# Kernel optimization log

Measured on AMD Instinct MI355X. Metric: run time of the kernel, lower is better.

The kernel has to match this reference:

```python
import jax, jax.numpy as jnp
import numpy as np
import math

N, B, C, H = 197, 256, 768, 12
HEAD = C // H
DROP_RATE = 0.5  # forward-arg drop_rate, hardcoded (float scalar)


def setup_inputs() -> dict:
    key = jax.random.key(0)
    ks = jax.random.split(key, 6)
    s = lambda k, shape: jax.random.normal(k, shape, jnp.float32) * 0.02
    return dict(
        x=jax.random.normal(ks[0], (N, B, C), jnp.float32),
        ln1_g=jnp.ones((C,), jnp.float32), ln1_b=jnp.zeros((C,), jnp.float32),
        in_proj_w=s(ks[1], (3 * C, C)), in_proj_b=jnp.zeros((3 * C,), jnp.float32),
        out_proj_w=s(ks[2], (C, C)), out_proj_b=jnp.zeros((C,), jnp.float32),
        ln2_g=jnp.ones((C,), jnp.float32), ln2_b=jnp.zeros((C,), jnp.float32),
        fc_w=s(ks[3], (4 * C, C)), fc_b=jnp.zeros((4 * C,), jnp.float32),
        proj_w=s(ks[4], (C, 4 * C)), proj_b=jnp.zeros((C,), jnp.float32),
    )


def layernorm(x, g, b, eps=1e-5):
    x32 = x.astype(jnp.float32)
    mu = x32.mean(-1, keepdims=True)
    var = x32.var(-1, keepdims=True)
    return ((x32 - mu) * jax.lax.rsqrt(var + eps) * g + b).astype(x.dtype)


def quick_gelu(x):
    return x * jax.nn.sigmoid(1.702 * x)


def mha(x, w, b, ow, ob):
    # x: (N, B, C); torch nn.MultiheadAttention with need_weights=True,
    # average_attn_weights=False -> weights (B, H, N, N)
    qkv = jnp.einsum('nbc,dc->nbd', x, w) + b
    q, k, v = jnp.split(qkv, 3, axis=-1)
    heads = lambda t: t.reshape(t.shape[0], B, H, HEAD).transpose(1, 2, 0, 3)  # (B,H,N,hd)
    q, k, v = heads(q), heads(k), heads(v)
    scale = 1.0 / np.sqrt(HEAD).astype(np.float32)
    scores = jnp.einsum('bhqd,bhkd->bhqk', q, k) * scale
    attn_w = jax.nn.softmax(scores, axis=-1)  # (B, H, N, N)
    o = jnp.einsum('bhqk,bhkd->bhqd', attn_w, v)
    o = o.transpose(2, 0, 1, 3).reshape(x.shape[0], B, C)
    return jnp.einsum('nbc,dc->nbd', o, ow) + ob, attn_w


def evit_block(x, ln1_g, ln1_b, in_proj_w, in_proj_b, out_proj_w, out_proj_b,
               ln2_g, ln2_b, fc_w, fc_b, proj_w, proj_b):
    L = math.ceil((1.0 - DROP_RATE) * (N - 1))  # left_tokens
    tmp, attn_w = mha(layernorm(x, ln1_g, ln1_b), in_proj_w, in_proj_b, out_proj_w, out_proj_b)
    x = x + tmp
    cls_attn = attn_w[:, :, 0, 1:].mean(axis=1)  # (B, N-1): CLS->patch attn, head-avg
    _, idx = jax.lax.top_k(cls_attn, L)          # (B, L), sorted descending like torch.topk
    nb = x[1:].transpose(1, 0, 2)                # (B, N-1, C) non-cls tokens, batch-first
    x_others = jnp.take_along_axis(nb, idx[:, :, None], axis=1)  # (B, L, C)
    # complement_idx: arange, zero out topk positions, sort, drop first L entries
    a = jnp.broadcast_to(jnp.arange(N - 1), (B, N - 1))
    mask = jnp.zeros((B, N - 1), bool).at[jnp.arange(B)[:, None], idx].set(True)
    compl = jnp.sort(jnp.where(mask, 0, a), axis=1)[:, L:]       # (B, N-1-L)
    non_topk = jnp.take_along_axis(nb, compl[:, :, None], axis=1)      # (B, M, C)
    non_topk_attn = jnp.take_along_axis(cls_attn, compl, axis=1)       # (B, M)
    extra = jnp.sum(non_topk * non_topk_attn[:, :, None], axis=1)      # (B, C) weighted merge
    x_new = jnp.concatenate([x[:1], x_others.transpose(1, 0, 2), extra[None]], axis=0)  # (L+2,B,C)
    h = layernorm(x_new, ln2_g, ln2_b)
    h = quick_gelu(jnp.einsum('nbc,fc->nbf', h, fc_w) + fc_b)
    h = jnp.einsum('nbf,cf->nbc', h, proj_w) + proj_b
    return x_new + h


def reference(x, ln1_g, ln1_b, in_proj_w, in_proj_b, out_proj_w, out_proj_b,
              ln2_g, ln2_b, fc_w, fc_b, proj_w, proj_b):
    return evit_block(x, ln1_g, ln1_b, in_proj_w, in_proj_b, out_proj_w, out_proj_b,
                      ln2_g, ln2_b, fc_w, fc_b, proj_w, proj_b)
```

## Files before the change

### kernel.cpp

```cpp
#include <hip/hip_runtime.h>
#include <math.h>

#define NT   197
#define BB   256
#define CD   768
#define NHD  12
#define HD   64
#define LTK  98
#define NEWN 100
#define M1   (NT*BB)
#define M2   (NEWN*BB)

typedef __attribute__((ext_vector_type(8))) short short8;
typedef __attribute__((ext_vector_type(4))) float float4v;

__device__ __forceinline__ short f2bf(float f) {
    unsigned int u = __float_as_uint(f);
    u = (u + 0x7fffu + ((u >> 16) & 1u)) >> 16;
    return (short)u;
}

__device__ __forceinline__ void global_to_lds16(const short* g, short* l) {
    __builtin_amdgcn_global_load_lds(
        (__attribute__((address_space(1))) void*)(void*)g,
        (__attribute__((address_space(3))) void*)l, 16, 0, 0);
}

__global__ __launch_bounds__(256) void cvt_bf16(const float* __restrict__ s,
                                                short* __restrict__ d, int n) {
    int i = blockIdx.x * 256 + threadIdx.x;
    if (i < n) d[i] = f2bf(s[i]);
}

__global__ __launch_bounds__(256)
void ln_fwd(const float* __restrict__ x, const float* __restrict__ g,
            const float* __restrict__ bb, short* __restrict__ ob,
            float2* __restrict__ stats) {
    int row = blockIdx.x * 4 + (threadIdx.x >> 6);
    int lane = threadIdx.x & 63;
    const float* xr = x + (size_t)row * CD;
    float v[12]; float s = 0.f;
#pragma unroll
    for (int i = 0; i < 12; i++) { v[i] = xr[lane + i * 64]; s += v[i]; }
#pragma unroll
    for (int o = 32; o; o >>= 1) s += __shfl_xor(s, o);
    float mu = s * (1.f / 768.f);
    float s2 = 0.f;
#pragma unroll
    for (int i = 0; i < 12; i++) { float d = v[i] - mu; s2 += d * d; }
#pragma unroll
    for (int o = 32; o; o >>= 1) s2 += __shfl_xor(s2, o);
    float rsig = rsqrtf(s2 * (1.f / 768.f) + 1e-5f);
    if (stats != nullptr && lane == 0) stats[row] = make_float2(mu, rsig);
#pragma unroll
    for (int i = 0; i < 12; i++) {
        int c = lane + i * 64;
        ob[(size_t)row * CD + c] = f2bf((v[i] - mu) * rsig * g[c] + bb[c]);
    }
}

template <int EPI>
__global__ __launch_bounds__(512)
void gemm_bt(const short* __restrict__ A, const short* __restrict__ Bw,
             const float* __restrict__ bias, const float* __restrict__ res,
             void* __restrict__ out, int M, int Nd, int K) {
    __shared__ short As[256 * 32];
    __shared__ short Bs[128 * 32];
    const int tid = threadIdx.x;

    const int mTiles = M >> 8, nTiles = Nd >> 7;
    const int GM = 8;
    int per = GM * nTiles;
    int grp = blockIdx.x / per;
    int rem = blockIdx.x - grp * per;
    int gm = mTiles - grp * GM; if (gm > GM) gm = GM;
    int mt = grp * GM + rem % gm;
    int nt = rem / gm;
    const int m0 = mt * 256, n0 = nt * 128;

    const int wave = tid >> 6, lane = tid & 63;
    const int wm = wave >> 1, wn = wave & 1;

    float4v acc[4][4];
#pragma unroll
    for (int a = 0; a < 4; a++)
#pragma unroll
        for (int b = 0; b < 4; b++) acc[a][b] = (float4v){0.f, 0.f, 0.f, 0.f};

    const int r = lane & 15, q = lane >> 4;

    for (int k0 = 0; k0 < K; k0 += 32) {
#pragma unroll
        for (int i = 0; i < 2; i++) {
            int id = (wave * 2 + i) * 64 + lane;
            int row = id >> 2, cpos = id & 3;
            int csrc = cpos ^ ((row >> 1) & 3);
            global_to_lds16(A + (size_t)(m0 + row) * K + k0 + csrc * 8,
                            As + (wave * 2 + i) * 512);
        }
        {
            int id = wave * 64 + lane;
            int row = id >> 2, cpos = id & 3;
            int csrc = cpos ^ ((row >> 1) & 3);
            global_to_lds16(Bw + (size_t)(n0 + row) * K + k0 + csrc * 8,
                            Bs + wave * 512);
        }
        __syncthreads();
        short8 af[4], bf[4];
#pragma unroll
        for (int mi = 0; mi < 4; mi++) {
            int row = wm * 64 + mi * 16 + r;
            int cp = q ^ ((row >> 1) & 3);
            af[mi] = *(const short8*)(As + row * 32 + cp * 8);
        }
#pragma unroll
        for (int ni = 0; ni < 4; ni++) {
            int row = wn * 64 + ni * 16 + r;
            int cp = q ^ ((row >> 1) & 3);
            bf[ni] = *(const short8*)(Bs + row * 32 + cp * 8);
        }
#pragma unroll
        for (int mi = 0; mi < 4; mi++)
#pragma unroll
            for (int ni = 0; ni < 4; ni++)
                acc[mi][ni] = __builtin_amdgcn_mfma_f32_16x16x32_bf16(
                    af[mi], bf[ni], acc[mi][ni], 0, 0, 0);
        __syncthreads();
    }

#pragma unroll
    for (int ni = 0; ni < 4; ni++) {
        int col = n0 + wn * 64 + ni * 16 + r;
        float bv = bias[col];
#pragma unroll
        for (int mi = 0; mi < 4; mi++) {
#pragma unroll
            for (int r2 = 0; r2 < 4; r2++) {
                int row = m0 + wm * 64 + mi * 16 + q * 4 + r2;
                size_t off = (size_t)row * Nd + col;
                float v = acc[mi][ni][r2] + bv;
                if (EPI == 0) {
                    ((short*)out)[off] = f2bf(v);
                } else if (EPI == 1) {
                    ((float*)out)[off] = v + res[off];
                } else {
                    float gel = v / (1.f + __expf(-1.702f * v));
                    ((short*)out)[off] = f2bf(gel);
                }
            }
        }
    }
}

__global__ __launch_bounds__(448)
void attn_kernel(const short* __restrict__ qkv, short* __restrict__ o) {
    __shared__ short Ks[224 * 72];
    __shared__ short Vt[64 * 232];
    __shared__ short Ps[7 * 16 * 232];

    const int b = blockIdx.x / NHD, h = blockIdx.x % NHD;
    const int tid = threadIdx.x;
    const int wave = tid >> 6, lane = tid & 63;

#pragma unroll
    for (int i = 0; i < 4; i++) {
        int id = tid + 448 * i;
        int n = id >> 3, ch = id & 7;
        uint4 val = {0u, 0u, 0u, 0u};
        if (n < NT)
            val = *(const uint4*)(qkv + ((size_t)(n * BB + b) * 2304 + 768 + h * 64 + ch * 8));
        *(uint4*)(&Ks[n * 72 + ch * 8]) = val;
    }
#pragma unroll
    for (int rr = 0; rr < 8; rr++) {
        int p = (tid >> 5) + rr * 14;
        int dl = tid & 31;
        int n0p = 2 * p;
#pragma unroll
        for (int di = 0; di < 2; di++) {
            int d = dl + 32 * di;
            unsigned int pack = 0;
            if (n0p < NT)
                pack |= (unsigned int)*(const unsigned short*)(qkv +
                    ((size_t)(n0p * BB + b) * 2304 + 1536 + h * 64 + d));
            if (n0p + 1 < NT)
                pack |= ((unsigned int)*(const unsigned short*)(qkv +
                    ((size_t)((n0p + 1) * BB + b) * 2304 + 1536 + h * 64 + d))) << 16;
            *(unsigned int*)(&Vt[d * 232 + n0p]) = pack;
        }
    }
    __syncthreads();

    short* Ps_w = Ps + wave * 16 * 232;
    const int cl = lane & 15, qg = lane >> 4;

    for (int rep = 0; rep < 2; rep++) {
        int qt = wave + rep * 7;
        int q0 = qt * 16;
        int m = q0 + cl; int mrow = (m < NT) ? m : (NT - 1);
        short8 qf[2];
#pragma unroll
        for (int kk = 0; kk < 2; kk++)
            qf[kk] = *(const short8*)(qkv + ((size_t)(mrow * BB + b) * 2304 +
                                             h * 64 + kk * 32 + qg * 8));
        float4v sacc[14];
#pragma unroll
        for (int nt = 0; nt < 14; nt++) sacc[nt] = (float4v){0.f, 0.f, 0.f, 0.f};
#pragma unroll
        for (int kk = 0; kk < 2; kk++) {
#pragma unroll
            for (int nt = 0; nt < 14; nt++) {
                short8 kf = *(const short8*)(&Ks[(nt * 16 + cl) * 72 + kk * 32 + qg * 8]);
                sacc[nt] = __builtin_amdgcn_mfma_f32_16x16x32_bf16(qf[kk], kf, sacc[nt], 0, 0, 0);
            }
        }
        float mx[4] = {-1e30f, -1e30f, -1e30f, -1e30f};
#pragma unroll
        for (int nt = 0; nt < 14; nt++) {
            int col = nt * 16 + cl;
            bool valid = col < NT;
#pragma unroll
            for (int r2 = 0; r2 < 4; r2++) {
                if (!valid) sacc[nt][r2] = -1e30f;
                mx[r2] = fmaxf(mx[r2], sacc[nt][r2]);
            }
        }
#pragma unroll
        for (int o2 = 1; o2 < 16; o2 <<= 1)
#pragma unroll
            for (int r2 = 0; r2 < 4; r2++) mx[r2] = fmaxf(mx[r2], __shfl_xor(mx[r2], o2));
        float sm[4] = {0.f, 0.f, 0.f, 0.f};
#pragma unroll
        for (int nt = 0; nt < 14; nt++)
#pragma unroll
            for (int r2 = 0; r2 < 4; r2++) {
                float pv = __expf((sacc[nt][r2] - mx[r2]) * 0.125f);
                sacc[nt][r2] = pv; sm[r2] += pv;
            }
#pragma unroll
        for (int o2 = 1; o2 < 16; o2 <<= 1)
#pragma unroll
            for (int r2 = 0; r2 < 4; r2++) sm[r2] += __shfl_xor(sm[r2], o2);
        float inv[4];
#pragma unroll
        for (int r2 = 0; r2 < 4; r2++) inv[r2] = 1.f / sm[r2];
#pragma unroll
        for (int nt = 0; nt < 14; nt++) {
            int col = nt * 16 + cl;
#pragma unroll
            for (int r2 = 0; r2 < 4; r2++)
                Ps_w[(qg * 4 + r2) * 232 + col] = f2bf(sacc[nt][r2] * inv[r2]);
        }
        __syncthreads();
        float4v oacc[4];
#pragma unroll
        for (int dt = 0; dt < 4; dt++) oacc[dt] = (float4v){0.f, 0.f, 0.f, 0.f};
#pragma unroll
        for (int kk = 0; kk < 7; kk++) {
            short8 pf = *(const short8*)(&Ps_w[cl * 232 + kk * 32 + qg * 8]);
#pragma unroll
            for (int dt = 0; dt < 4; dt++) {
                short8 vf = *(const short8*)(&Vt[(dt * 16 + cl) * 232 + kk * 32 + qg * 8]);
                oacc[dt] = __builtin_amdgcn_mfma_f32_16x16x32_bf16(pf, vf, oacc[dt], 0, 0, 0);
            }
        }
#pragma unroll
        for (int dt = 0; dt < 4; dt++)
#pragma unroll
            for (int r2 = 0; r2 < 4; r2++) {
                int qrow = q0 + qg * 4 + r2;
                if (qrow < NT)
                    o[((size_t)qrow * BB + b) * CD + h * 64 + dt * 16 + cl] = f2bf(oacc[dt][r2]);
            }
        __syncthreads();
    }
}

__global__ __launch_bounds__(256)
void u_kernel(const float* __restrict__ x, const float2* __restrict__ stats,
              const float* __restrict__ g, const float* __restrict__ bln,
              const float* __restrict__ W, const float* __restrict__ pb,
              float* __restrict__ u, float* __restrict__ tq) {
    int b = blockIdx.x;
    __shared__ float lncls[CD];
    __shared__ float qc[CD];
    float2 st = stats[b];
    for (int c = threadIdx.x; c < CD; c += 256)
        lncls[c] = (x[(size_t)b * CD + c] - st.x) * st.y * g[c] + bln[c];
    __syncthreads();
    for (int d = threadIdx.x; d < CD; d += 256) {
        const float* wr = W + (size_t)d * CD;
        float acc = 0.f;
        for (int c = 0; c < CD; c++) acc += wr[c] * lncls[c];
        qc[d] = acc + pb[d];
    }
    __syncthreads();
    for (int t = threadIdx.x; t < NHD * CD; t += 256) {
        int h = t / CD, c = t % CD;
        const float* wk = W + (size_t)(CD + h * 64) * CD + c;
        float acc = 0.f;
        for (int d = 0; d < 64; d++) acc += qc[h * 64 + d] * wk[(size_t)d * CD];
        u[((size_t)b * NHD + h) * CD + c] = acc;
    }
    if (threadIdx.x < NHD) {
        int h = threadIdx.x; float acc = 0.f;
        for (int d = 0; d < 64; d++) acc += qc[h * 64 + d] * pb[CD + h * 64 + d];
        tq[b * NHD + h] = acc;
    }
}

__global__ __launch_bounds__(256)
void scores_kernel(const float* __restrict__ x, const float2* __restrict__ stats,
                   const float* __restrict__ g, const float* __restrict__ bln,
                   const float* __restrict__ u, const float* __restrict__ tq,
                   float* __restrict__ scores) {
    int bi = blockIdx.x; int b = bi / NT, n = bi % NT;
    __shared__ float ln[CD];
    int row = n * BB + b;
    float2 st = stats[row];
    for (int c = threadIdx.x; c < CD; c += 256)
        ln[c] = (x[(size_t)row * CD + c] - st.x) * st.y * g[c] + bln[c];
    __syncthreads();
    int wave = threadIdx.x >> 6, lane = threadIdx.x & 63;
    for (int h = wave; h < NHD; h += 4) {
        const float* ub = u + ((size_t)b * NHD + h) * CD;
        float acc = 0.f;
#pragma unroll
        for (int i = 0; i < 12; i++) acc += ub[lane + i * 64] * ln[lane + i * 64];
#pragma unroll
        for (int o2 = 32; o2; o2 >>= 1) acc += __shfl_xor(acc, o2);
        if (lane == 0)
            scores[((size_t)b * NHD + h) * NT + n] = (acc + tq[b * NHD + h]) * 0.125f;
    }
}

__global__ __launch_bounds__(256)
void softmax_avg(const float* __restrict__ scores, float* __restrict__ cls_attn) {
    int b = blockIdx.x;
    __shared__ float p[NHD][NT];
    int wave = threadIdx.x >> 6, lane = threadIdx.x & 63;
    for (int h = wave; h < NHD; h += 4) {
        const float* s = scores + ((size_t)b * NHD + h) * NT;
        float v[4]; float mx = -1e30f;
#pragma unroll
        for (int i = 0; i < 4; i++) {
            int n = lane + i * 64;
            v[i] = (n < NT) ? s[n] : -1e30f;
            mx = fmaxf(mx, v[i]);
        }
#pragma unroll
        for (int o2 = 32; o2; o2 >>= 1) mx = fmaxf(mx, __shfl_xor(mx, o2));
        float sum = 0.f;
#pragma unroll
        for (int i = 0; i < 4; i++) {
            int n = lane + i * 64;
            v[i] = (n < NT) ? __expf(v[i] - mx) : 0.f;
            sum += v[i];
        }
#pragma unroll
        for (int o2 = 32; o2; o2 >>= 1) sum += __shfl_xor(sum, o2);
        float inv = 1.f / sum;
#pragma unroll
        for (int i = 0; i < 4; i++) {
            int n = lane + i * 64;
            if (n < NT) p[h][n] = v[i] * inv;
        }
    }
    __syncthreads();
    for (int n = 1 + (int)threadIdx.x; n < NT; n += 256) {
        float a = 0.f;
#pragma unroll
        for (int h = 0; h < NHD; h++) a += p[h][n];
        cls_attn[(size_t)b * (NT - 1) + n - 1] = a * (1.f / 12.f);
    }
}

__global__ __launch_bounds__(256)
void topk_kernel(const float* __restrict__ cls_attn, int* __restrict__ idx,
                 int* __restrict__ cidx, float* __restrict__ cw) {
    int b = blockIdx.x, t = threadIdx.x;
    __shared__ float kv[256];
    __shared__ int ki[256];
    __shared__ int pos[256];
    __shared__ unsigned char mem[256];
    float myv = (t < NT - 1) ? cls_attn[(size_t)b * (NT - 1) + t] : -INFINITY;
    kv[t] = myv; ki[t] = t;
    __syncthreads();
    for (int k = 2; k <= 256; k <<= 1) {
        for (int j = k >> 1; j > 0; j >>= 1) {
            int ixj = t ^ j;
            if (ixj > t) {
                bool up = ((t & k) == 0);
                float va = kv[t], vb = kv[ixj];
                int ia = ki[t], ib = ki[ixj];
                bool beforeAB = (va > vb) || (va == vb && ia < ib);
                bool sw = up ? !beforeAB : beforeAB;
                if (sw) { kv[t] = vb; kv[ixj] = va; ki[t] = ib; ki[ixj] = ia; }
            }
            __syncthreads();
        }
    }
    if (t < LTK) idx[(size_t)b * LTK + t] = ki[t];
    mem[t] = 0;
    __syncthreads();
    if (t < LTK) mem[ki[t]] = 1;
    __syncthreads();
    int f = (t < NT - 1) ? (1 - (int)mem[t]) : 0;
    pos[t] = f;
    __syncthreads();
    for (int o2 = 1; o2 < 256; o2 <<= 1) {
        int add = (t >= o2) ? pos[t - o2] : 0;
        __syncthreads();
        pos[t] += add;
        __syncthreads();
    }
    if (f) {
        int p = pos[t] - 1;
        cidx[(size_t)b * LTK + p] = t;
        cw[(size_t)b * LTK + p] = myv;
    }
}

__global__ __launch_bounds__(256)
void assemble(const float* __restrict__ x1, const int* __restrict__ idx,
              const int* __restrict__ cidx, const float* __restrict__ cw,
              float* __restrict__ xnew) {
    int b = blockIdx.x;
    for (int c = threadIdx.x; c < CD; c += 256)
        xnew[(size_t)b * CD + c] = x1[(size_t)b * CD + c];
    for (int j = 0; j < LTK; j++) {
        int ns = idx[b * LTK + j] + 1;
        for (int c = threadIdx.x; c < CD; c += 256)
            xnew[((size_t)(1 + j) * BB + b) * CD + c] = x1[((size_t)ns * BB + b) * CD + c];
    }
    float acc[3] = {0.f, 0.f, 0.f};
    for (int m = 0; m < LTK; m++) {
        int ns = cidx[b * LTK + m] + 1;
        float w = cw[b * LTK + m];
#pragma unroll
        for (int i = 0; i < 3; i++)
            acc[i] += w * x1[((size_t)ns * BB + b) * CD + threadIdx.x + i * 256];
    }
#pragma unroll
    for (int i = 0; i < 3; i++)
        xnew[((size_t)99 * BB + b) * CD + threadIdx.x + i * 256] = acc[i];
}

__global__ __launch_bounds__(256) void sentinel_fill(float* __restrict__ p, int n) {
    int i = blockIdx.x * 256 + threadIdx.x;
    if (i < n) p[i] = 12345.0f;
}

#define OFF_WQKVB 0ULL
#define OFF_WOB   3538944ULL
#define OFF_WFCB  4718592ULL
#define OFF_WPRB  9437184ULL
#define OFF_STATS 14155776ULL
#define OFF_LN1   14559232ULL
#define OFF_O     OFF_LN1
#define OFF_QKV   92022784ULL
#define OFF_H     OFF_QKV
#define OFF_X1    324413440ULL
#define OFF_U     479340544ULL
#define OFF_TQ    488777728ULL
#define OFF_SC    488790016ULL
#define OFF_CA    491210752ULL
#define OFF_IDX   491411456ULL
#define OFF_CIDX  491511808ULL
#define OFF_CW    491612160ULL
#define OFF_XNEW  491712512ULL
#define OFF_LN2   570355712ULL
#define WS_NEED   609677312ULL

extern "C" void kernel_launch(void* const* d_in, const int* in_sizes, int n_in,
                              void* d_out, int out_size, void* d_ws, size_t ws_size,
                              hipStream_t stream) {
    const float* x      = (const float*)d_in[0];
    const float* ln1_g  = (const float*)d_in[1];
    const float* ln1_b  = (const float*)d_in[2];
    const float* w_qkv  = (const float*)d_in[3];
    const float* b_qkv  = (const float*)d_in[4];
    const float* w_o    = (const float*)d_in[5];
    const float* b_o    = (const float*)d_in[6];
    const float* ln2_g  = (const float*)d_in[7];
    const float* ln2_b  = (const float*)d_in[8];
    const float* w_fc   = (const float*)d_in[9];
    const float* b_fc   = (const float*)d_in[10];
    const float* w_proj = (const float*)d_in[11];
    const float* b_proj = (const float*)d_in[12];

    if (ws_size < WS_NEED) {
        sentinel_fill<<<(out_size + 255) / 256, 256, 0, stream>>>((float*)d_out, out_size);
        return;
    }

    char* ws = (char*)d_ws;
    short*  W_QKVB = (short*)(ws + OFF_WQKVB);
    short*  W_OB   = (short*)(ws + OFF_WOB);
    short*  W_FCB  = (short*)(ws + OFF_WFCB);
    short*  W_PRB  = (short*)(ws + OFF_WPRB);
    float2* STATS  = (float2*)(ws + OFF_STATS);
    short*  LN1    = (short*)(ws + OFF_LN1);
    short*  O      = (short*)(ws + OFF_O);
    short*  QKV    = (short*)(ws + OFF_QKV);
    short*  H      = (short*)(ws + OFF_H);
    float*  X1     = (float*)(ws + OFF_X1);
    float*  U      = (float*)(ws + OFF_U);
    float*  TQ     = (float*)(ws + OFF_TQ);
    float*  SC     = (float*)(ws + OFF_SC);
    float*  CA     = (float*)(ws + OFF_CA);
    int*    IDX    = (int*)(ws + OFF_IDX);
    int*    CIDX   = (int*)(ws + OFF_CIDX);
    float*  CW     = (float*)(ws + OFF_CW);
    float*  XNEW   = (float*)(ws + OFF_XNEW);
    short*  LN2    = (short*)(ws + OFF_LN2);

    cvt_bf16<<<(2304 * 768 + 255) / 256, 256, 0, stream>>>(w_qkv, W_QKVB, 2304 * 768);
    cvt_bf16<<<(768 * 768 + 255) / 256, 256, 0, stream>>>(w_o, W_OB, 768 * 768);
    cvt_bf16<<<(3072 * 768 + 255) / 256, 256, 0, stream>>>(w_fc, W_FCB, 3072 * 768);
    cvt_bf16<<<(768 * 3072 + 255) / 256, 256, 0, stream>>>(w_proj, W_PRB, 768 * 3072);

    ln_fwd<<<M1 / 4, 256, 0, stream>>>(x, ln1_g, ln1_b, LN1, STATS);

    gemm_bt<0><<<(M1 / 256) * (2304 / 128), 512, 0, stream>>>(
        LN1, W_QKVB, b_qkv, nullptr, QKV, M1, 2304, 768);

    attn_kernel<<<BB * NHD, 448, 0, stream>>>(QKV, O);

    u_kernel<<<BB, 256, 0, stream>>>(x, STATS, ln1_g, ln1_b, w_qkv, b_qkv, U, TQ);
    scores_kernel<<<BB * NT, 256, 0, stream>>>(x, STATS, ln1_g, ln1_b, U, TQ, SC);
    softmax_avg<<<BB, 256, 0, stream>>>(SC, CA);
    topk_kernel<<<BB, 256, 0, stream>>>(CA, IDX, CIDX, CW);

    gemm_bt<1><<<(M1 / 256) * (768 / 128), 512, 0, stream>>>(
        O, W_OB, b_o, x, X1, M1, 768, 768);

    assemble<<<BB, 256, 0, stream>>>(X1, IDX, CIDX, CW, XNEW);

    ln_fwd<<<M2 / 4, 256, 0, stream>>>(XNEW, ln2_g, ln2_b, LN2, nullptr);

    gemm_bt<2><<<(M2 / 256) * (3072 / 128), 512, 0, stream>>>(
        LN2, W_FCB, b_fc, nullptr, H, M2, 3072, 768);

    gemm_bt<1><<<(M2 / 256) * (768 / 128), 512, 0, stream>>>(
        H, W_PRB, b_proj, XNEW, (float*)d_out, M2, 768, 3072);
}
```

Measured before the change: 1.863 ms.

## Batch CLS-query projections as tiled GEMMs and use 128-tile GEMM for final projection

The per-batch u_kernel, which ran a naive 768x768 matvec and a per-head projection with one block per batch element, is split into an LN kernel plus two shared-memory tiled fp32 GEMMs and a small tq kernel. The weight matrix is now read once per tile instead of once per batch element. The final MLP down-projection moves to a new 128x128-tile GEMM with 256 threads, giving more blocks for the small M2 problem. The cost is more kernel launches and extra intermediate buffers that alias the X1 workspace region.

Result: faster. 1.669 ms (-10.4%).

```diff
diff --git a/kernel.cpp b/kernel.cpp
--- a/kernel.cpp
+++ b/kernel.cpp
@@ -152,6 +152,94 @@
     }
 }
 
+template <int EPI>
+__global__ __launch_bounds__(256)
+void gemm_bt128(const short* __restrict__ A, const short* __restrict__ Bw,
+                const float* __restrict__ bias, const float* __restrict__ res,
+                void* __restrict__ out, int M, int Nd, int K) {
+    __shared__ short As[128 * 32];
+    __shared__ short Bs[128 * 32];
+    const int tid = threadIdx.x;
+
+    const int mTiles = M >> 7, nTiles = Nd >> 7;
+    const int GM = 8;
+    int per = GM * nTiles;
+    int grp = blockIdx.x / per;
+    int rem = blockIdx.x - grp * per;
+    int gm = mTiles - grp * GM; if (gm > GM) gm = GM;
+    int mt = grp * GM + rem % gm;
+    int nt = rem / gm;
+    const int m0 = mt * 128, n0 = nt * 128;
+
+    const int wave = tid >> 6, lane = tid & 63;
+    const int wm = wave >> 1, wn = wave & 1;
+
+    float4v acc[4][4];
+#pragma unroll
+    for (int a = 0; a < 4; a++)
+#pragma unroll
+        for (int b = 0; b < 4; b++) acc[a][b] = (float4v){0.f, 0.f, 0.f, 0.f};
+
+    const int r = lane & 15, q = lane >> 4;
+
+    for (int k0 = 0; k0 < K; k0 += 32) {
+#pragma unroll
+        for (int i = 0; i < 2; i++) {
+            int id = (wave * 2 + i) * 64 + lane;
+            int row = id >> 2, cpos = id & 3;
+            int csrc = cpos ^ ((row >> 1) & 3);
+            global_to_lds16(A + (size_t)(m0 + row) * K + k0 + csrc * 8,
+                            As + (wave * 2 + i) * 512);
+            global_to_lds16(Bw + (size_t)(n0 + row) * K + k0 + csrc * 8,
+                            Bs + (wave * 2 + i) * 512);
+        }
+        __syncthreads();
+        short8 af[4], bf[4];
+#pragma unroll
+        for (int mi = 0; mi < 4; mi++) {
+            int row = wm * 64 + mi * 16 + r;
+            int cp = q ^ ((row >> 1) & 3);
+            af[mi] = *(const short8*)(As + row * 32 + cp * 8);
+        }
+#pragma unroll
+        for (int ni = 0; ni < 4; ni++) {
+            int row = wn * 64 + ni * 16 + r;
+            int cp = q ^ ((row >> 1) & 3);
+            bf[ni] = *(const short8*)(Bs + row * 32 + cp * 8);
+        }
+#pragma unroll
+        for (int mi = 0; mi < 4; mi++)
+#pragma unroll
+            for (int ni = 0; ni < 4; ni++)
+                acc[mi][ni] = __builtin_amdgcn_mfma_f32_16x16x32_bf16(
+                    af[mi], bf[ni], acc[mi][ni], 0, 0, 0);
+        __syncthreads();
+    }
+
+#pragma unroll
+    for (int ni = 0; ni < 4; ni++) {
+        int col = n0 + wn * 64 + ni * 16 + r;
+        float bv = bias[col];
+#pragma unroll
+        for (int mi = 0; mi < 4; mi++) {
+#pragma unroll
+            for (int r2 = 0; r2 < 4; r2++) {
+                int row = m0 + wm * 64 + mi * 16 + q * 4 + r2;
+                size_t off = (size_t)row * Nd + col;
+                float v = acc[mi][ni][r2] + bv;
+                if (EPI == 0) {
+                    ((short*)out)[off] = f2bf(v);
+                } else if (EPI == 1) {
+                    ((float*)out)[off] = v + res[off];
+                } else {
+                    float gel = v / (1.f + __expf(-1.702f * v));
+                    ((short*)out)[off] = f2bf(gel);
+                }
+            }
+        }
+    }
+}
+
 __global__ __launch_bounds__(448)
 void attn_kernel(const short* __restrict__ qkv, short* __restrict__ o) {
     __shared__ short Ks[224 * 72];
@@ -276,37 +364,117 @@
     }
 }
 
-__global__ __launch_bounds__(256)
-void u_kernel(const float* __restrict__ x, const float2* __restrict__ stats,
-              const float* __restrict__ g, const float* __restrict__ bln,
-              const float* __restrict__ W, const float* __restrict__ pb,
-              float* __restrict__ u, float* __restrict__ tq) {
+
+__global__ __launch_bounds__(256)
+void lnc_kernel(const float* __restrict__ x, const float2* __restrict__ stats,
+                const float* __restrict__ g, const float* __restrict__ bln,
+                float* __restrict__ lnc) {
     int b = blockIdx.x;
-    __shared__ float lncls[CD];
-    __shared__ float qc[CD];
     float2 st = stats[b];
-    for (int c = threadIdx.x; c < CD; c += 256)
-        lncls[c] = (x[(size_t)b * CD + c] - st.x) * st.y * g[c] + bln[c];
-    __syncthreads();
-    for (int d = threadIdx.x; d < CD; d += 256) {
-        const float* wr = W + (size_t)d * CD;
-        float acc = 0.f;
-        for (int c = 0; c < CD; c++) acc += wr[c] * lncls[c];
-        qc[d] = acc + pb[d];
-    }
-    __syncthreads();
-    for (int t = threadIdx.x; t < NHD * CD; t += 256) {
-        int h = t / CD, c = t % CD;
-        const float* wk = W + (size_t)(CD + h * 64) * CD + c;
-        float acc = 0.f;
-        for (int d = 0; d < 64; d++) acc += qc[h * 64 + d] * wk[(size_t)d * CD];
-        u[((size_t)b * NHD + h) * CD + c] = acc;
-    }
-    if (threadIdx.x < NHD) {
-        int h = threadIdx.x; float acc = 0.f;
-        for (int d = 0; d < 64; d++) acc += qc[h * 64 + d] * pb[CD + h * 64 + d];
-        tq[b * NHD + h] = acc;
-    }
+#pragma unroll
+    for (int i = 0; i < 3; i++) {
+        int c = threadIdx.x + i * 256;
+        lnc[(size_t)b * CD + c] = (x[(size_t)b * CD + c] - st.x) * st.y * g[c] + bln[c];
+    }
+}
+
+__global__ __launch_bounds__(256)
+void gemm32_nt(const float* __restrict__ A, const float* __restrict__ B,
+               const float* __restrict__ bias, float* __restrict__ C,
+               int lda, int ldb, int ldc) {
+    __shared__ float As[32][65];
+    __shared__ float Bs[32][65];
+    const int tid = threadIdx.x;
+    const int m0 = blockIdx.x * 64, n0 = blockIdx.y * 64;
+    const int tx = tid & 15, ty = tid >> 4;
+    float acc[4][4] = {};
+    const int K = 768;
+    for (int k0 = 0; k0 < K; k0 += 32) {
+#pragma unroll
+        for (int i = 0; i < 8; i++) {
+            int idx = i * 256 + tid;
+            int rr = idx >> 5, kc = idx & 31;
+            As[kc][rr] = A[(size_t)(m0 + rr) * lda + k0 + kc];
+            Bs[kc][rr] = B[(size_t)(n0 + rr) * ldb + k0 + kc];
+        }
+        __syncthreads();
+#pragma unroll
+        for (int kk = 0; kk < 32; kk++) {
+            float a_[4], b_[4];
+#pragma unroll
+            for (int i = 0; i < 4; i++) a_[i] = As[kk][ty * 4 + i];
+#pragma unroll
+            for (int j = 0; j < 4; j++) b_[j] = Bs[kk][tx * 4 + j];
+#pragma unroll
+            for (int i = 0; i < 4; i++)
+#pragma unroll
+                for (int j = 0; j < 4; j++) acc[i][j] += a_[i] * b_[j];
+        }
+        __syncthreads();
+    }
+#pragma unroll
+    for (int i = 0; i < 4; i++)
+#pragma unroll
+        for (int j = 0; j < 4; j++) {
+            int n = n0 + tx * 4 + j;
+            C[(size_t)(m0 + ty * 4 + i) * ldc + n] = acc[i][j] + bias[n];
+        }
+}
+
+__global__ __launch_bounds__(256)
+void gemm32_nn_u(const float* __restrict__ QC, const float* __restrict__ W,
+                 float* __restrict__ U) {
+    __shared__ float As[32][65];
+    __shared__ float Bs[32][65];
+    const int tid = threadIdx.x;
+    const int m0 = blockIdx.x * 64, n0 = blockIdx.y * 64, h = blockIdx.z;
+    const float* A = QC + h * 64;
+    const float* B = W + (size_t)(CD + h * 64) * CD;
+    const int tx = tid & 15, ty = tid >> 4;
+    float acc[4][4] = {};
+    for (int k0 = 0; k0 < 64; k0 += 32) {
+#pragma unroll
+        for (int i = 0; i < 8; i++) {
+            int idx = i * 256 + tid;
+            int mr = idx >> 5, kc = idx & 31;
+            As[kc][mr] = A[(size_t)(m0 + mr) * CD + k0 + kc];
+            int kr = idx >> 6, nc = idx & 63;
+            if (i < 8) {  }
+            Bs[kr][nc] = B[(size_t)(k0 + kr) * CD + n0 + nc];
+        }
+        __syncthreads();
+#pragma unroll
+        for (int kk = 0; kk < 32; kk++) {
+            float a_[4], b_[4];
+#pragma unroll
+            for (int i = 0; i < 4; i++) a_[i] = As[kk][ty * 4 + i];
+#pragma unroll
+            for (int j = 0; j < 4; j++) b_[j] = Bs[kk][tx * 4 + j];
+#pragma unroll
+            for (int i = 0; i < 4; i++)
+#pragma unroll
+                for (int j = 0; j < 4; j++) acc[i][j] += a_[i] * b_[j];
+        }
+        __syncthreads();
+    }
+#pragma unroll
+    for (int i = 0; i < 4; i++)
+#pragma unroll
+        for (int j = 0; j < 4; j++) {
+            int b = m0 + ty * 4 + i, c = n0 + tx * 4 + j;
+            U[((size_t)b * NHD + h) * CD + c] = acc[i][j];
+        }
+}
+
+__global__ __launch_bounds__(256)
+void tq_kernel(const float* __restrict__ QC, const float* __restrict__ pb,
+               float* __restrict__ tq) {
+    int h = blockIdx.x, b = threadIdx.x;
+    float acc = 0.f;
+#pragma unroll
+    for (int d = 0; d < 64; d++)
+        acc += QC[(size_t)b * CD + h * 64 + d] * pb[CD + h * 64 + d];
+    tq[b * NHD + h] = acc;
 }
 
 __global__ __launch_bounds__(256)
@@ -461,6 +629,8 @@
 #define OFF_QKV   92022784ULL
 #define OFF_H     OFF_QKV
 #define OFF_X1    324413440ULL
+#define OFF_LNC   OFF_X1
+#define OFF_QC    (OFF_X1 + 786432ULL)
 #define OFF_U     479340544ULL
 #define OFF_TQ    488777728ULL
 #define OFF_SC    488790016ULL
@@ -505,6 +675,8 @@
     short*  QKV    = (short*)(ws + OFF_QKV);
     short*  H      = (short*)(ws + OFF_H);
     float*  X1     = (float*)(ws + OFF_X1);
+    float*  LNC    = (float*)(ws + OFF_LNC);
+    float*  QC     = (float*)(ws + OFF_QC);
     float*  U      = (float*)(ws + OFF_U);
     float*  TQ     = (float*)(ws + OFF_TQ);
     float*  SC     = (float*)(ws + OFF_SC);
@@ -527,7 +699,11 @@
 
     attn_kernel<<<BB * NHD, 448, 0, stream>>>(QKV, O);
 
-    u_kernel<<<BB, 256, 0, stream>>>(x, STATS, ln1_g, ln1_b, w_qkv, b_qkv, U, TQ);
+    lnc_kernel<<<BB, 256, 0, stream>>>(x, STATS, ln1_g, ln1_b, LNC);
+    gemm32_nt<<<dim3(BB / 64, CD / 64), 256, 0, stream>>>(
+        LNC, w_qkv, b_qkv, QC, CD, CD, CD);
+    gemm32_nn_u<<<dim3(BB / 64, CD / 64, NHD), 256, 0, stream>>>(QC, w_qkv, U);
+    tq_kernel<<<NHD, 256, 0, stream>>>(QC, b_qkv, TQ);
     scores_kernel<<<BB * NT, 256, 0, stream>>>(x, STATS, ln1_g, ln1_b, U, TQ, SC);
     softmax_avg<<<BB, 256, 0, stream>>>(SC, CA);
     topk_kernel<<<BB, 256, 0, stream>>>(CA, IDX, CIDX, CW);
@@ -542,6 +718,6 @@
     gemm_bt<2><<<(M2 / 256) * (3072 / 128), 512, 0, stream>>>(
         LN2, W_FCB, b_fc, nullptr, H, M2, 3072, 768);
 
-    gemm_bt<1><<<(M2 / 256) * (768 / 128), 512, 0, stream>>>(
+    gemm_bt128<1><<<(M2 / 128) * (768 / 128), 256, 0, stream>>>(
         H, W_PRB, b_proj, XNEW, (float*)d_out, M2, 768, 3072);
 }
```
